# Optimization experiments

Hardware: AMD Instinct MI355X
Metric: run time of the kernel (lower is better)

Reference implementation:

```python
import jax, jax.numpy as jnp
import numpy as np

NODES = 23   # 22 players + ball per frame-graph
K = 8        # random neighbors per node
B, T = 64, 128
G = B * T            # total graphs (frames)
N = G * NODES        # total nodes
D_IN, H, RH = 16, 128, 128


def setup_inputs() -> dict:
    key = jax.random.key(0)
    ks = jax.random.split(key, 10)
    x = jax.random.normal(ks[0], (N, D_IN), jnp.float32)
    # per-graph random edges: dst = each node repeated K times, src = random node in same graph
    src_local = jax.random.randint(ks[1], (G, NODES * K), 0, NODES)
    dst_local = jnp.tile(jnp.repeat(jnp.arange(NODES), K)[None, :], (G, 1))
    off = (jnp.arange(G) * NODES)[:, None]
    edge_index = jnp.stack([(src_local + off).reshape(-1),
                            (dst_local + off).reshape(-1)]).astype(jnp.int32)
    runner_idx = jax.random.randint(ks[2], (G,), 0, NODES, dtype=jnp.int32)
    sc = lambda k, sh: (jax.random.normal(k, sh, jnp.float32) * 0.05)
    return {
        'x': x, 'edge_index': edge_index, 'runner_idx': runner_idx,
        'W1': sc(ks[3], (D_IN, H)), 'b1': jnp.zeros((H,), jnp.float32),
        'W2': sc(ks[4], (H, H)),    'b2': jnp.zeros((H,), jnp.float32),
        'W_ih': sc(ks[5], (3 * RH, H)), 'W_hh': sc(ks[6], (3 * RH, RH)),
        'b_ih': jnp.zeros((3 * RH,), jnp.float32), 'b_hh': jnp.zeros((3 * RH,), jnp.float32),
        'Wp': sc(ks[7], (RH, 2)), 'bp': jnp.zeros((2,), jnp.float32),
    }


def _gcn_conv(h, edge_index, W, b):
    # PyG GCNConv: add self-loops, symmetric normalization, scatter-sum
    h = h @ W
    loop = jnp.arange(N, dtype=edge_index.dtype)
    s = jnp.concatenate([edge_index[0], loop])
    d = jnp.concatenate([edge_index[1], loop])
    deg = jax.ops.segment_sum(jnp.ones_like(s, h.dtype), d, num_segments=N)
    dinv = jnp.where(deg > 0, jax.lax.rsqrt(deg), 0.0)
    norm = dinv[s] * dinv[d]                      # [E+N]
    out = jax.ops.segment_sum(h[s] * norm[:, None], d, num_segments=N)
    return out + b


def _gru(seq, W_ih, W_hh, b_ih, b_hh):
    # torch GRU: gates in r,z,n order
    xg = seq @ W_ih.T + b_ih                      # [B,T,3RH]
    def step(hprev, xt):
        gh = hprev @ W_hh.T + b_hh
        xr, xz, xn = jnp.split(xt, 3, axis=-1)
        hr, hz, hn = jnp.split(gh, 3, axis=-1)
        r = jax.nn.sigmoid(xr + hr)
        z = jax.nn.sigmoid(xz + hz)
        n = jnp.tanh(xn + r * hn)
        hnew = (1.0 - z) * n + z * hprev
        return hnew, hnew
    h0 = jnp.zeros((seq.shape[0], RH), seq.dtype)
    _, outs = jax.lax.scan(step, h0, jnp.swapaxes(xg, 0, 1))
    return jnp.swapaxes(outs, 0, 1)               # [B,T,RH]


def reference(x, edge_index, runner_idx, W1, b1, W2, b2,
              W_ih, W_hh, b_ih, b_hh, Wp, bp):
    h = jax.nn.relu(_gcn_conv(x, edge_index, W1, b1))
    h = jax.nn.relu(_gcn_conv(h, edge_index, W2, b2))
    # fused equivalent of the per-graph nonzero()/indexing loop:
    runner_global = jnp.arange(G, dtype=jnp.int32) * NODES + runner_idx
    seq = h[runner_global].reshape(B, T, H)       # all lengths == T, padding is a no-op
    out = _gru(seq, W_ih, W_hh, b_ih, b_hh)
    return out @ Wp + bp                          # [B,T,2]
```

## Files before the change

kernel.cpp:

```cpp
#include <hip/hip_runtime.h>
#include <hip/hip_bf16.h>
#include <math.h>

#define GG 8192
#define NODESN 23
#define KK 8
#define DIN 16
#define HH 128
#define RHH 128
#define EPG (NODESN*KK)
#define TTT 128
#define BBB 64
#define HPAD 132

#define GRU_BARRIER() asm volatile("s_waitcnt lgkmcnt(0)\n\ts_barrier" ::: "memory")

__global__ __launch_bounds__(256) void gcn_hsum(
    const float* __restrict__ x, const int* __restrict__ esrc,
    const int* __restrict__ runner,
    const float* __restrict__ W1, const float* __restrict__ b1,
    float* __restrict__ hsum_g)
{
    __shared__ float xs[NODESN * DIN];
    __shared__ int   srcs[EPG];
    __shared__ float t1[NODESN * HH];
    __shared__ float red[256];

    const int g   = blockIdx.x;
    const int tid = threadIdx.x;
    const int j   = tid & 127;
    const int nh  = tid >> 7;

    for (int i = tid; i < NODESN * DIN; i += 256) xs[i] = x[g * NODESN * DIN + i];
    for (int i = tid; i < EPG; i += 256)          srcs[i] = esrc[g * EPG + i] - g * NODESN;

    float w[DIN];
    #pragma unroll
    for (int k = 0; k < DIN; k++) w[k] = W1[k * HH + j];
    const float b1j = b1[j];
    __syncthreads();

    const int n0 = nh * 12;
    const int n1 = nh ? NODESN : 12;
    for (int n = n0; n < n1; n++) {
        float acc = 0.f;
        #pragma unroll
        for (int k = 0; k < DIN; k += 4) {
            float4 xv = *(const float4*)&xs[n * DIN + k];
            acc = fmaf(xv.x, w[k], fmaf(xv.y, w[k+1], fmaf(xv.z, w[k+2], fmaf(xv.w, w[k+3], acc))));
        }
        t1[n * HH + j] = acc;
    }
    __syncthreads();

    const int r = runner[g];
    float part = 0.f;
    for (int slot = nh; slot < 9; slot += 2) {
        int node = (slot < 8) ? srcs[r * KK + slot] : r;
        float acc = t1[node * HH + j];
        #pragma unroll
        for (int k = 0; k < KK; k++) acc += t1[srcs[node * KK + k] * HH + j];
        part += fmaxf(acc * (1.f / 9.f) + b1j, 0.f);
    }
    red[tid] = part;
    __syncthreads();
    if (tid < HH) hsum_g[(size_t)g * HH + tid] = red[tid] + red[tid + 128];
}

__global__ __launch_bounds__(256) void seq_kernel(
    const float* __restrict__ hsum_g, const float* __restrict__ W2,
    const float* __restrict__ b2, float* __restrict__ seq)
{
    __shared__ float hs[16 * HH];
    const int tid = threadIdx.x;
    const int j = tid & 127, mh = tid >> 7;
    const size_t base = (size_t)blockIdx.x * 16 * HH;

    for (int v = tid; v < 16 * HH / 4; v += 256)
        ((float4*)hs)[v] = ((const float4*)(hsum_g + base))[v];
    __syncthreads();

    float acc[8];
    #pragma unroll
    for (int m = 0; m < 8; m++) acc[m] = 0.f;
    const float* hrow = hs + mh * 8 * HH;
    for (int k = 0; k < HH; k += 4) {
        float w0  = W2[(k+0)*HH + j];
        float w1  = W2[(k+1)*HH + j];
        float w2v = W2[(k+2)*HH + j];
        float w3  = W2[(k+3)*HH + j];
        #pragma unroll
        for (int m = 0; m < 8; m++) {
            float4 hv = *(const float4*)&hrow[m * HH + k];
            acc[m] = fmaf(hv.x, w0, fmaf(hv.y, w1, fmaf(hv.z, w2v, fmaf(hv.w, w3, acc[m]))));
        }
    }
    const float bj = b2[j];
    #pragma unroll
    for (int m = 0; m < 8; m++)
        seq[base + (size_t)(mh * 8 + m) * HH + j] = fmaxf(acc[m] * (1.f/9.f) + bj, 0.f);
}

__global__ void transpose_wih(const float* __restrict__ W, float* __restrict__ WT)
{
    int idx = blockIdx.x * 256 + threadIdx.x;
    if (idx < 3 * RHH * RHH) {
        int jj = idx / RHH, kk = idx - jj * RHH;
        WT[kk * (3 * RHH) + jj] = W[idx];
    }
}

__global__ __launch_bounds__(384) void xg_kernel(
    const float* __restrict__ seq, const float* __restrict__ WT,
    const float* __restrict__ b_ih, float* __restrict__ xg)
{
    const int tid = threadIdx.x;
    const int m0 = blockIdx.x * 8;
    const float* srow = seq + (size_t)m0 * RHH;
    float acc[8];
    const float bv = b_ih[tid];
    #pragma unroll
    for (int mi = 0; mi < 8; mi++) acc[mi] = bv;
    for (int k = 0; k < RHH; k += 4) {
        float w0 = WT[(k+0)*384 + tid];
        float w1 = WT[(k+1)*384 + tid];
        float w2 = WT[(k+2)*384 + tid];
        float w3 = WT[(k+3)*384 + tid];
        #pragma unroll
        for (int mi = 0; mi < 8; mi++) {
            float4 sv = *(const float4*)(srow + mi * RHH + k);
            acc[mi] = fmaf(sv.x, w0, fmaf(sv.y, w1, fmaf(sv.z, w2, fmaf(sv.w, w3, acc[mi]))));
        }
    }
    #pragma unroll
    for (int mi = 0; mi < 8; mi++)
        xg[(size_t)(m0 + mi) * 384 + tid] = acc[mi];
}

__global__ __launch_bounds__(1024, 4) void gru_kernel(
    const float* __restrict__ xg, const float* __restrict__ W_hh,
    const float* __restrict__ b_hh, const float* __restrict__ Wp,
    const float* __restrict__ bp, float* __restrict__ out)
{
    __shared__ float h_hist[(TTT + 1) * HPAD];
    __shared__ float xg_s[2][3 * RHH];

    const int b   = blockIdx.x;
    const int tid = threadIdx.x;
    const int i   = tid >> 3;
    const int q   = tid & 7;

    float wr[16], wz[16], wn[16];
    int loff[4];
    {
        const float* br = W_hh + (size_t)i * RHH;
        const float* bz = br + (size_t)RHH * RHH;
        const float* bn = bz + (size_t)RHH * RHH;
        #pragma unroll
        for (int m = 0; m < 4; m++) {
            int p = (m + (q >> 1)) & 3;
            int o = q * 16 + 4 * p;
            loff[m] = o;
            float4 v;
            v = *(const float4*)(br + o); wr[4*m]=v.x; wr[4*m+1]=v.y; wr[4*m+2]=v.z; wr[4*m+3]=v.w;
            v = *(const float4*)(bz + o); wz[4*m]=v.x; wz[4*m+1]=v.y; wz[4*m+2]=v.z; wz[4*m+3]=v.w;
            v = *(const float4*)(bn + o); wn[4*m]=v.x; wn[4*m+1]=v.y; wn[4*m+2]=v.z; wn[4*m+3]=v.w;
        }
    }
    #pragma unroll
    for (int m = 0; m < 16; m++) {
        asm volatile("" : "+v"(wr[m]));
        asm volatile("" : "+v"(wz[m]));
        asm volatile("" : "+v"(wn[m]));
    }

    float bhr = 0.f, bhz = 0.f, bhn = 0.f;
    if (q == 0) { bhr = b_hh[i]; bhz = b_hh[RHH + i]; bhn = b_hh[2 * RHH + i]; }

    if (tid < RHH) h_hist[tid] = 0.f;
    const float* xbase = xg + (size_t)b * TTT * 3 * RHH;
    float xnext = 0.f;
    if (tid < 3 * RHH) {
        xg_s[0][tid] = xbase[tid];
        xnext = xbase[3 * RHH + tid];
    }
    float hprev = 0.f;
    __syncthreads();

    for (int t = 0; t < TTT; t++) {
        const float* hrow = &h_hist[t * HPAD];
        float ar = 0.f, az = 0.f, an = 0.f;
        #pragma unroll
        for (int m = 0; m < 4; m++) {
            float4 hv = *(const float4*)(hrow + loff[m]);
            ar = fmaf(hv.x, wr[4*m], fmaf(hv.y, wr[4*m+1], fmaf(hv.z, wr[4*m+2], fmaf(hv.w, wr[4*m+3], ar))));
            az = fmaf(hv.x, wz[4*m], fmaf(hv.y, wz[4*m+1], fmaf(hv.z, wz[4*m+2], fmaf(hv.w, wz[4*m+3], az))));
            an = fmaf(hv.x, wn[4*m], fmaf(hv.y, wn[4*m+1], fmaf(hv.z, wn[4*m+2], fmaf(hv.w, wn[4*m+3], an))));
        }

        if (tid < 3 * RHH) {
            xg_s[(t + 1) & 1][tid] = xnext;
            xnext = (t + 2 < TTT) ? xbase[(size_t)(t + 2) * 3 * RHH + tid] : 0.f;
        }

        ar += __shfl_xor(ar, 1); ar += __shfl_xor(ar, 2); ar += __shfl_xor(ar, 4);
        az += __shfl_xor(az, 1); az += __shfl_xor(az, 2); az += __shfl_xor(az, 4);
        an += __shfl_xor(an, 1); an += __shfl_xor(an, 2); an += __shfl_xor(an, 4);

        if (q == 0) {
            const float* xr_s = xg_s[t & 1];
            float xr = xr_s[i], xz = xr_s[RHH + i], xn = xr_s[2 * RHH + i];
            float sr = xr + ar + bhr;
            float sz = xz + az + bhz;
            float rg = 1.f / (1.f + __expf(-sr));
            float zg = 1.f / (1.f + __expf(-sz));
            float tv = fmaf(rg, an + bhn, xn);
            tv = fminf(fmaxf(tv, -15.f), 15.f);
            float e2 = __expf(-2.f * tv);
            float ng = (1.f - e2) / (1.f + e2);
            hprev = fmaf(zg, hprev, (1.f - zg) * ng);
            h_hist[(t + 1) * HPAD + i] = hprev;
        }
        GRU_BARRIER();
    }

    if (tid < 2 * RHH) xg_s[0][tid] = Wp[tid];
    if (tid < 2)       xg_s[1][tid] = bp[tid];
    __syncthreads();

    {
        const int s = tid & 3;
        const int c = (tid >> 2) & 1;
        const int t = tid >> 3;
        float acc = 0.f;
        const float* hr = &h_hist[(t + 1) * HPAD + s * 32];
        #pragma unroll
        for (int ii = 0; ii < 32; ii += 4) {
            float4 hv = *(const float4*)(hr + ii);
            int k = s * 32 + ii;
            acc = fmaf(hv.x, xg_s[0][(k+0)*2 + c],
                  fmaf(hv.y, xg_s[0][(k+1)*2 + c],
                  fmaf(hv.z, xg_s[0][(k+2)*2 + c],
                  fmaf(hv.w, xg_s[0][(k+3)*2 + c], acc))));
        }
        acc += __shfl_xor(acc, 1);
        acc += __shfl_xor(acc, 2);
        if (s == 0)
            out[((size_t)b * TTT + t) * 2 + c] = acc + xg_s[1][c];
    }
}

extern "C" void kernel_launch(void* const* d_in, const int* in_sizes, int n_in,
                              void* d_out, int out_size, void* d_ws, size_t ws_size,
                              hipStream_t stream)
{
    const float* x      = (const float*)d_in[0];
    const int*   eidx   = (const int*)d_in[1];
    const int*   runner = (const int*)d_in[2];
    const float* W1     = (const float*)d_in[3];
    const float* b1     = (const float*)d_in[4];
    const float* W2     = (const float*)d_in[5];
    const float* b2     = (const float*)d_in[6];
    const float* W_ih   = (const float*)d_in[7];
    const float* W_hh   = (const float*)d_in[8];
    const float* b_ih   = (const float*)d_in[9];
    const float* b_hh   = (const float*)d_in[10];
    const float* Wp     = (const float*)d_in[11];
    const float* bp     = (const float*)d_in[12];
    float* out = (float*)d_out;

    float* seq    = (float*)d_ws;
    float* xg     = seq + (size_t)GG * HH;
    float* WT     = xg + (size_t)GG * 3 * RHH;
    float* hsum_g = xg;

    transpose_wih<<<192, 256, 0, stream>>>(W_ih, WT);
    gcn_hsum<<<GG, 256, 0, stream>>>(x, eidx, runner, W1, b1, hsum_g);
    seq_kernel<<<GG / 16, 256, 0, stream>>>(hsum_g, W2, b2, seq);
    xg_kernel<<<GG / 8, 384, 0, stream>>>(seq, WT, b_ih, xg);
    gru_kernel<<<BBB, 1024, 0, stream>>>(xg, W_hh, b_hh, Wp, bp, out);
}
```

Baseline: 264.9 us.

## Split GRU output projection into separate kernel and shrink GRU shared memory

The GRU kernel no longer keeps the full hidden-state history in LDS. It uses a two-row ping-pong buffer and writes each hidden state to global memory (reusing the seq buffer). A new proj_kernel applies the Wp/bp projection over all rows in parallel. The launch bounds change to amdgpu_waves_per_eu(4,4) and the asm register pinning is dropped, which changes how the compiler allocates the weight registers in the serial loop. The cost is an extra kernel launch and a global write/read of the hidden states.

```diff
diff --git a/kernel.cpp b/kernel.cpp
--- a/kernel.cpp
+++ b/kernel.cpp
@@ -11,7 +11,6 @@
 #define EPG (NODESN*KK)
 #define TTT 128
 #define BBB 64
-#define HPAD 132
 
 #define GRU_BARRIER() asm volatile("s_waitcnt lgkmcnt(0)\n\ts_barrier" ::: "memory")
 
@@ -137,12 +136,13 @@
         xg[(size_t)(m0 + mi) * 384 + tid] = acc[mi];
 }
 
-__global__ __launch_bounds__(1024, 4) void gru_kernel(
+__global__ __launch_bounds__(1024)
+__attribute__((amdgpu_waves_per_eu(4, 4)))
+void gru_kernel(
     const float* __restrict__ xg, const float* __restrict__ W_hh,
-    const float* __restrict__ b_hh, const float* __restrict__ Wp,
-    const float* __restrict__ bp, float* __restrict__ out)
-{
-    __shared__ float h_hist[(TTT + 1) * HPAD];
+    const float* __restrict__ b_hh, float* __restrict__ h_out)
+{
+    __shared__ float hbuf[2][HH];
     __shared__ float xg_s[2][3 * RHH];
 
     const int b   = blockIdx.x;
@@ -167,17 +167,11 @@
             v = *(const float4*)(bn + o); wn[4*m]=v.x; wn[4*m+1]=v.y; wn[4*m+2]=v.z; wn[4*m+3]=v.w;
         }
     }
-    #pragma unroll
-    for (int m = 0; m < 16; m++) {
-        asm volatile("" : "+v"(wr[m]));
-        asm volatile("" : "+v"(wz[m]));
-        asm volatile("" : "+v"(wn[m]));
-    }
 
     float bhr = 0.f, bhz = 0.f, bhn = 0.f;
     if (q == 0) { bhr = b_hh[i]; bhz = b_hh[RHH + i]; bhn = b_hh[2 * RHH + i]; }
 
-    if (tid < RHH) h_hist[tid] = 0.f;
+    if (tid < HH) hbuf[0][tid] = 0.f;
     const float* xbase = xg + (size_t)b * TTT * 3 * RHH;
     float xnext = 0.f;
     if (tid < 3 * RHH) {
@@ -185,10 +179,11 @@
         xnext = xbase[3 * RHH + tid];
     }
     float hprev = 0.f;
+    float* hob = h_out + (size_t)b * TTT * HH;
     __syncthreads();
 
     for (int t = 0; t < TTT; t++) {
-        const float* hrow = &h_hist[t * HPAD];
+        const float* hrow = hbuf[t & 1];
         float ar = 0.f, az = 0.f, an = 0.f;
         #pragma unroll
         for (int m = 0; m < 4; m++) {
@@ -219,34 +214,41 @@
             float e2 = __expf(-2.f * tv);
             float ng = (1.f - e2) / (1.f + e2);
             hprev = fmaf(zg, hprev, (1.f - zg) * ng);
-            h_hist[(t + 1) * HPAD + i] = hprev;
+            hbuf[(t + 1) & 1][i] = hprev;
+            hob[t * HH + i] = hprev;
         }
         GRU_BARRIER();
     }
-
-    if (tid < 2 * RHH) xg_s[0][tid] = Wp[tid];
-    if (tid < 2)       xg_s[1][tid] = bp[tid];
-    __syncthreads();
-
-    {
-        const int s = tid & 3;
-        const int c = (tid >> 2) & 1;
-        const int t = tid >> 3;
-        float acc = 0.f;
-        const float* hr = &h_hist[(t + 1) * HPAD + s * 32];
-        #pragma unroll
-        for (int ii = 0; ii < 32; ii += 4) {
-            float4 hv = *(const float4*)(hr + ii);
-            int k = s * 32 + ii;
-            acc = fmaf(hv.x, xg_s[0][(k+0)*2 + c],
-                  fmaf(hv.y, xg_s[0][(k+1)*2 + c],
-                  fmaf(hv.z, xg_s[0][(k+2)*2 + c],
-                  fmaf(hv.w, xg_s[0][(k+3)*2 + c], acc))));
-        }
-        acc += __shfl_xor(acc, 1);
-        acc += __shfl_xor(acc, 2);
-        if (s == 0)
-            out[((size_t)b * TTT + t) * 2 + c] = acc + xg_s[1][c];
+}
+
+__global__ __launch_bounds__(256) void proj_kernel(
+    const float* __restrict__ h_out, const float* __restrict__ Wp,
+    const float* __restrict__ bp, float* __restrict__ out)
+{
+    __shared__ float wps[2 * RHH];
+    __shared__ float bps[2];
+    const int tid = threadIdx.x;
+    if (tid < 2 * RHH) wps[tid] = Wp[tid];
+    if (tid < 2) bps[tid] = bp[tid];
+    __syncthreads();
+
+    const int s = tid & 7;
+    const int rl = tid >> 3;
+    const size_t row = (size_t)blockIdx.x * 32 + rl;
+    const float* hr = h_out + row * HH + s * 16;
+    float a0 = 0.f, a1 = 0.f;
+    #pragma unroll
+    for (int m = 0; m < 16; m += 4) {
+        float4 hv = *(const float4*)(hr + m);
+        int k = s * 16 + m;
+        a0 = fmaf(hv.x, wps[(k+0)*2], fmaf(hv.y, wps[(k+1)*2], fmaf(hv.z, wps[(k+2)*2], fmaf(hv.w, wps[(k+3)*2], a0))));
+        a1 = fmaf(hv.x, wps[(k+0)*2+1], fmaf(hv.y, wps[(k+1)*2+1], fmaf(hv.z, wps[(k+2)*2+1], fmaf(hv.w, wps[(k+3)*2+1], a1))));
+    }
+    a0 += __shfl_xor(a0, 1); a0 += __shfl_xor(a0, 2); a0 += __shfl_xor(a0, 4);
+    a1 += __shfl_xor(a1, 1); a1 += __shfl_xor(a1, 2); a1 += __shfl_xor(a1, 4);
+    if (s == 0) {
+        out[row * 2 + 0] = a0 + bps[0];
+        out[row * 2 + 1] = a1 + bps[1];
     }
 }
 
@@ -273,10 +275,12 @@
     float* xg     = seq + (size_t)GG * HH;
     float* WT     = xg + (size_t)GG * 3 * RHH;
     float* hsum_g = xg;
+    float* h_out  = seq;
 
     transpose_wih<<<192, 256, 0, stream>>>(W_ih, WT);
     gcn_hsum<<<GG, 256, 0, stream>>>(x, eidx, runner, W1, b1, hsum_g);
     seq_kernel<<<GG / 16, 256, 0, stream>>>(hsum_g, W2, b2, seq);
     xg_kernel<<<GG / 8, 384, 0, stream>>>(seq, WT, b_ih, xg);
-    gru_kernel<<<BBB, 1024, 0, stream>>>(xg, W_hh, b_hh, Wp, bp, out);
-}
+    gru_kernel<<<BBB, 1024, 0, stream>>>(xg, W_hh, b_hh, h_out);
+    proj_kernel<<<GG / 32, 256, 0, stream>>>(h_out, Wp, bp, out);
+}
```

New measurement: 280.3 us. 1.06x slower.
